# Optimization experiments

Measured on AMD Instinct MI355X. Metric: run time of the kernel, lower is better.

## Reference

```python
import jax, jax.numpy as jnp
import numpy as np

SR = 44100.0
J, Q = 12, 16
W0 = 2.0 * np.pi      # MorletWavelet.freq_to_w_at_s(1.0, s=1.0) -> w = 2*pi*f*s
N_SIG = 3.0           # wavelet support = +/- N_SIG standard deviations


def _make_wavelet_bank():
    """Morlet filter bank: J octaves, Q steps/octave, highest freq = nyquist.
    Returns centered, zero-padded real/imag filter stacks of shape (K, Lmax)."""
    dt = 1.0 / SR
    nyq = SR / 2.0
    wavelets = []
    for j in range(J):
        for q in range(Q):
            f = nyq / (2.0 ** (j + q / Q))
            s = 1.0 / f                      # center freq f = W0/(2*pi*s) = 1/s
            M = int(np.ceil(N_SIG * s * SR))  # half support in samples
            t = np.arange(-M, M + 1) * dt
            psi = (np.pi ** -0.25) / np.sqrt(s) \
                * np.exp(1j * W0 * t / s) * np.exp(-0.5 * (t / s) ** 2)
            psi = psi / np.sum(np.abs(psi))   # L1 normalization
            wavelets.append(psi.astype(np.complex64))
    Lmax = max(len(p) for p in wavelets)       # odd (2*M_max + 1)
    bank = np.zeros((len(wavelets), Lmax), np.complex64)
    for i, p in enumerate(wavelets):
        left = (Lmax - len(p)) // 2            # center-pad each wavelet
        bank[i, left:left + len(p)] = p
    return bank


def setup_inputs() -> dict:
    key = jax.random.key(0)
    x = jax.random.normal(key, (2, 1, 32768), dtype=jnp.float32)
    bank = _make_wavelet_bank()
    return {
        "x": x,
        "filt_real": jnp.asarray(bank.real, dtype=jnp.float32),
        "filt_imag": jnp.asarray(bank.imag, dtype=jnp.float32),
    }


def _scat1d(x, filt_real, filt_imag):
    # x: (B, 1, T); filters: (K, L) with L odd. Equivalent to the torch path:
    # pad input by L//2, cross-correlate (F.conv1d) with each complex wavelet,
    # take the modulus. Done via FFT (same math, efficient for ~47k-tap kernels).
    K, L = filt_real.shape
    B, C, T = x.shape  # C == 1 (squeeze_channels=True)
    P = L // 2
    xp = jnp.pad(x[:, 0, :], ((0, 0), (P, P)))       # (B, T + 2P)
    n_full = xp.shape[-1] + L - 1
    N = 1 << (n_full - 1).bit_length()               # next pow2 FFT size
    X = jnp.fft.rfft(xp, N)                          # (B, N//2+1)
    Gr = jnp.fft.rfft(filt_real[:, ::-1], N)         # flip -> corr via conv
    Gi = jnp.fft.rfft(filt_imag[:, ::-1], N)         # (K, N//2+1)
    lo = L - 1                                       # valid-corr offset
    yr = jnp.fft.irfft(X[:, None, :] * Gr[None], N)[..., lo:lo + T]
    yi = jnp.fft.irfft(X[:, None, :] * Gi[None], N)[..., lo:lo + T]
    return jnp.sqrt(yr * yr + yi * yi)               # (B, K, T) modulus


def reference(x, filt_real, filt_imag):
    return _scat1d(x, filt_real, filt_imag)
```

## Files before the change

### kernel.cpp

```cpp
#include <hip/hip_runtime.h>
#include <math.h>

#define T_LEN   32768
#define NK      192
#define NB      2
#define KDIR    48
#define MAXM    56

struct SParams {
  int m1e[144];
  int voff[144];
  int slot[144];
  int ab[9];
  int jb[10];
};

__device__ __forceinline__ int j2_of_q(int q) {
  return 4 + (q >= 5) + (q >= 10) + (q >= 15);
}

__global__ __launch_bounds__(256) void k_vtab(float* __restrict__ ws, SParams P) {
  int ki = blockIdx.y;
  int slotc = P.slot[ki];
  int M1e = P.m1e[ki];
  float* dst = ws + P.voff[ki];
  int nent = 2 * M1e + 2;
  int k = ki + 48;
  int j = k >> 4, q = k & 15;
  float sig = 2.f * exp2f((float)(16 * j + q) * 0.0625f);
  float s1 = sig * 0.86602540378f;
  float gc = -0.5f / (s1 * s1);
  float om = 6.28318530718f / sig;
  float norm = 1.f / (2.50662827463f * s1 * erff((float)M1e / (1.41421356237f * s1)));
  #pragma unroll
  for (int e0 = 0; e0 < 4; ++e0) {
    int e = blockIdx.x * 1024 + e0 * 256 + threadIdx.x;
    if (e >= slotc) continue;
    if (e >= nent) { dst[2 * e] = 0.f; dst[2 * e + 1] = 0.f; continue; }
    float mm = (float)(e - M1e);
    float g = __expf(gc * mm * mm) * norm;
    float sn, cs; __sincosf(om * mm, &sn, &cs);
    dst[2 * e] = g * cs;
    dst[2 * e + 1] = g * sn;
  }
}

__global__ __launch_bounds__(256) void k_zero(float* __restrict__ ws, int base, int n) {
  int i = blockIdx.x * 256 + threadIdx.x;
  if (i < n) ws[base + i] = 0.f;
}


template<int J, int G, int S, int CH>
__device__ __forceinline__ void deep_path(const float* __restrict__ x,
                                          float* __restrict__ ws, const SParams& P,
                                          int q, int rc, int tid,
                                          float* xs, float* red) {
  constexpr int d = 1 << J;
  constexpr int E = 4096;
  constexpr int W = E + (G - 1) * d + 2;
  const int tile = rc / CH;
  const int chunk = rc % CH;
  const int ki = 16 * (J - 3) + q;
  const int J2 = j2_of_q(q);
  const int M1e = P.m1e[ki];
  const int slot = P.slot[ki];
  const int e_base = chunk * (S * E);
  if (e_base >= slot) return;
  const float* vt = ws + P.voff[ki];
  const int n0 = tile * G;
  const int ubase0 = (n0 - J2) * d - M1e;
  const float* xb0 = x;
  const float* xb1 = x + T_LEN;

  float acc[4 * G];
  #pragma unroll
  for (int i = 0; i < 4 * G; ++i) acc[i] = 0.f;

  #pragma unroll
  for (int s = 0; s < S; ++s) {
    int e0 = e_base + s * E;
    if (e0 >= slot) break;
    int ub = ubase0 + e0;
    if (ub >= T_LEN || ub + W <= 0) continue;
    int Ech = slot - e0; if (Ech > E) Ech = E;
    int Wn = Ech + (G - 1) * d + 2;
    int Wh = (Wn + 1) >> 1;
    for (int i = tid; i < Wh; i += 256) {
      int u0 = ub + 2 * i;
      bool ok = (unsigned)u0 <= (unsigned)(T_LEN - 2);
      int uc = ok ? u0 : 0;
      float2 a = *(const float2*)(xb0 + uc);
      float2 b = *(const float2*)(xb1 + uc);
      float4 w;
      w.x = ok ? a.x : 0.f; w.y = ok ? b.x : 0.f;
      w.z = ok ? a.y : 0.f; w.w = ok ? b.y : 0.f;
      *(float4*)(xs + 4 * i) = w;
    }
    __syncthreads();
    int pend = Ech >> 9;
    const float4* xp0 = (const float4*)xs + tid;
    const float* vte = vt + 2 * e0 + 4 * tid;
    for (int ps = 0; ps < pend; ++ps) {
      float4 v = *(const float4*)(vte + (ps << 10));
      const float4* xp = xp0 + (ps << 8);
      #pragma unroll
      for (int g = 0; g < G; ++g) {
        float4 xv = xp[g * (d >> 1)];
        acc[4 * g + 0] += v.x * xv.x + v.z * xv.z;
        acc[4 * g + 1] += v.y * xv.x + v.w * xv.z;
        acc[4 * g + 2] += v.x * xv.y + v.z * xv.w;
        acc[4 * g + 3] += v.y * xv.y + v.w * xv.w;
      }
    }
    __syncthreads();
  }

  #pragma unroll
  for (int st = 1; st < 64; st <<= 1) {
    #pragma unroll
    for (int i = 0; i < 4 * G; ++i) acc[i] += __shfl_xor(acc[i], st, 64);
  }
  int wv = tid >> 6;
  if ((tid & 63) == 0) {
    #pragma unroll
    for (int gg = 0; gg < G; ++gg)
      *(float4*)(red + wv * 64 + 4 * gg) =
        make_float4(acc[4 * gg], acc[4 * gg + 1], acc[4 * gg + 2], acc[4 * gg + 3]);
  }
  __syncthreads();
  if (tid < 4 * G)
    red[256 + tid] = red[tid] + red[64 + tid] + red[128 + tid] + red[192 + tid];
  __syncthreads();
  if (tid < G) {
    int nidx = n0 + tid;
    int Ncu = (32767 >> J) + 17;
    if (nidx < Ncu) {
      float ar0 = red[256 + 4 * tid], ai0 = red[256 + 4 * tid + 1];
      float ar1 = red[256 + 4 * tid + 2], ai1 = red[256 + 4 * tid + 3];
      float ndf = (float)((nidx - J2) * d);
      float rev = ndf * exp2f(-(float)(16 * (J + 1) + q) * 0.0625f);
      rev -= floorf(rev);
      float sn, cs; __sincosf(rev * 6.28318530718f, &sn, &cs);
      float* ap = ws + P.ab[J - 3] + (q * 2) * Ncu * 2;
      float r0 = ar0 * cs - ai0 * sn, i0 = ar0 * sn + ai0 * cs;
      float r1 = ar1 * cs - ai1 * sn, i1 = ar1 * sn + ai1 * cs;
      if (CH == 1) {
        *(float2*)(ap + 2 * nidx) = make_float2(r0, i0);
        *(float2*)(ap + 2 * (Ncu + nidx)) = make_float2(r1, i1);
      } else {
        atomicAdd(ap + 2 * nidx, r0);
        atomicAdd(ap + 2 * nidx + 1, i0);
        atomicAdd(ap + 2 * (Ncu + nidx), r1);
        atomicAdd(ap + 2 * (Ncu + nidx) + 1, i1);
      }
    }
  }
}

template<int J, int TOUT>
__device__ __forceinline__ void small_path(const float* __restrict__ x,
                                           float* __restrict__ ws, const SParams& P,
                                           int q, int tile, int tid,
                                           float* xs, float* red) {
  constexpr int d = 1 << J;
  const int ki = 16 * (J - 3) + q;
  const int J2 = j2_of_q(q);
  const int M1e = P.m1e[ki];
  const int nent = 2 * M1e + 2;
  const float* vt = ws + P.voff[ki];
  const int Ncu = (32767 >> J) + 17;
  const int o0 = tile * TOUT;
  const int ub = (o0 - J2) * d - M1e;
  const int W = (TOUT - 1) * d + nent;
  const int PS = W + (((W - 1) >> J) << 1) + 4;
  const float* xb0 = x;
  const float* xb1 = x + T_LEN;
  for (int i = tid; i < W; i += 256) {
    int u = ub + i;
    bool ok = (unsigned)u < (unsigned)T_LEN;
    int uc = ok ? u : 0;
    float a = xb0[uc]; a = ok ? a : 0.f;
    float bv = xb1[uc]; bv = ok ? bv : 0.f;
    int ad = i + ((i >> J) << 1);
    xs[ad] = a; xs[PS + ad] = bv;
  }
  __syncthreads();
  int th = (TOUT == 128) ? tid : (tid & 127);
  int o = th & (TOUT - 1);
  int b = th / TOUT;
  int half = (TOUT == 64) ? (tid >> 7) : 0;
  int e_lo = 0, e_hi = nent;
  if (TOUT == 64) {
    int eh = (nent >> 2) << 1;
    if (half) e_lo = eh; else e_hi = eh;
  }
  const float* pl = xs + b * PS;
  int sb = o * d;
  float ar = 0.f, ai = 0.f;
  #pragma unroll 4
  for (int e = e_lo; e < e_hi; e += 2) {
    float4 v = *(const float4*)(vt + 2 * e);
    int s = sb + e;
    float2 xv = *(const float2*)(pl + s + ((s >> J) << 1));
    ar += v.x * xv.x + v.z * xv.y;
    ai += v.y * xv.x + v.w * xv.y;
  }
  if (TOUT == 64) {
    if (tid >= 128) { red[2 * (tid - 128)] = ar; red[2 * (tid - 128) + 1] = ai; }
    __syncthreads();
    if (tid < 128) { ar += red[2 * tid]; ai += red[2 * tid + 1]; }
  }
  if (half == 0 && o0 + o < Ncu && (TOUT == 128 || tid < 128)) {
    int nidx = o0 + o;
    float ndf = (float)((nidx - J2) * d);
    float rev = ndf * exp2f(-(float)(16 * (J + 1) + q) * 0.0625f);
    rev -= floorf(rev);
    float sn, cs; __sincosf(rev * 6.28318530718f, &sn, &cs);
    float* ap = ws + P.ab[J - 3] + (q * 2) * Ncu * 2;
    *(float2*)(ap + 2 * (b * Ncu + nidx)) = make_float2(ar * cs - ai * sn, ar * sn + ai * cs);
  }
}

__global__ __launch_bounds__(256) void k_s1(const float* __restrict__ x,
                                            float* __restrict__ ws, SParams P) {
  __shared__ __align__(16) float xs[12292];
  __shared__ __align__(16) float red[512];
  int bx = blockIdx.x, tid = threadIdx.x;
  int o = 0;
  #pragma unroll
  for (int t = 1; t < 9; ++t) if (bx >= P.jb[t]) o = t;
  int j = 11 - o;
  int rem = bx - P.jb[o];
  int rc = rem >> 4, q = rem & 15;
  switch (j) {
    case 11: deep_path<11, 2, 2, 6>(x, ws, P, q, rc, tid, xs, red); break;
    case 10: deep_path<10, 3, 2, 3>(x, ws, P, q, rc, tid, xs, red); break;
    case 9:  deep_path<9, 4, 1, 3>(x, ws, P, q, rc, tid, xs, red); break;
    case 8:  deep_path<8, 8, 2, 1>(x, ws, P, q, rc, tid, xs, red); break;
    case 7:  deep_path<7, 16, 1, 1>(x, ws, P, q, rc, tid, xs, red); break;
    case 6:  small_path<6, 64>(x, ws, P, q, rc, tid, xs, red); break;
    case 5:  small_path<5, 128>(x, ws, P, q, rc, tid, xs, red); break;
    case 4:  small_path<4, 128>(x, ws, P, q, rc, tid, xs, red); break;
    default: small_path<3, 128>(x, ws, P, q, rc, tid, xs, red); break;
  }
}

__global__ __launch_bounds__(256) void k_stage2(const float* __restrict__ ws,
                                                float* __restrict__ out, SParams P) {
  int k = KDIR + blockIdx.y;
  int j = k >> 4, q = k & 15;
  int d = 1 << j;
  int J2 = j2_of_q(q);
  float sig = 2.f * exp2f((float)(16 * j + q) * 0.0625f);
  float s2 = sig * 0.5f;
  int Ncu = (32767 >> j) + 17;
  const float* A0 = ws + P.ab[j - 3] + (q * 2) * Ncu * 2;
  const float* A1 = A0 + Ncu * 2;
  int t0 = blockIdx.x * 256 + threadIdx.x;
  int phi = t0 & (d - 1);
  int nb0 = t0 >> j;
  int step = 8192 >> j;
  int ntap = 2 * J2 + 1;
  float fd = (float)d;
  float inv2 = 1.f / (s2 * s2);
  float u0 = (float)(phi + J2 * d);
  float eg = __expf(-0.5f * u0 * u0 * inv2);
  float mf = __expf((fd * u0 - 0.5f * fd * fd) * inv2);
  float qf = __expf(-fd * fd * inv2);
  float Z = 0.f;
  float sr0 = 0.f, si0 = 0.f, sr1 = 0.f, si1 = 0.f;
  float sr2 = 0.f, si2 = 0.f, sr3 = 0.f, si3 = 0.f;
  float tr0 = 0.f, ti0 = 0.f, tr1 = 0.f, ti1 = 0.f;
  float tr2 = 0.f, ti2 = 0.f, tr3 = 0.f, ti3 = 0.f;
  const float* Ap0 = A0 + 2 * nb0;
  const float* Ap1 = A1 + 2 * nb0;
  for (int rr = 0; rr < ntap; ++rr) {
    float w = eg; eg *= mf; mf *= qf; Z += w;
    float2 a0 = *(const float2*)(Ap0 + 2 * rr);
    float2 a1 = *(const float2*)(Ap0 + 2 * (rr + step));
    float2 a2 = *(const float2*)(Ap0 + 2 * (rr + 2 * step));
    float2 a3 = *(const float2*)(Ap0 + 2 * (rr + 3 * step));
    float2 b0 = *(const float2*)(Ap1 + 2 * rr);
    float2 b1 = *(const float2*)(Ap1 + 2 * (rr + step));
    float2 b2 = *(const float2*)(Ap1 + 2 * (rr + 2 * step));
    float2 b3 = *(const float2*)(Ap1 + 2 * (rr + 3 * step));
    sr0 += w * a0.x; si0 += w * a0.y; sr1 += w * a1.x; si1 += w * a1.y;
    sr2 += w * a2.x; si2 += w * a2.y; sr3 += w * a3.x; si3 += w * a3.y;
    tr0 += w * b0.x; ti0 += w * b0.y; tr1 += w * b1.x; ti1 += w * b1.y;
    tr2 += w * b2.x; ti2 += w * b2.y; tr3 += w * b3.x; ti3 += w * b3.y;
  }
  float zi = 1.f / Z;
  size_t ob0 = (size_t)k * T_LEN + t0;
  size_t ob1 = (size_t)(NK + k) * T_LEN + t0;
  out[ob0]         = sqrtf(sr0 * sr0 + si0 * si0) * zi;
  out[ob0 + 8192]  = sqrtf(sr1 * sr1 + si1 * si1) * zi;
  out[ob0 + 16384] = sqrtf(sr2 * sr2 + si2 * si2) * zi;
  out[ob0 + 24576] = sqrtf(sr3 * sr3 + si3 * si3) * zi;
  out[ob1]         = sqrtf(tr0 * tr0 + ti0 * ti0) * zi;
  out[ob1 + 8192]  = sqrtf(tr1 * tr1 + ti1 * ti1) * zi;
  out[ob1 + 16384] = sqrtf(tr2 * tr2 + ti2 * ti2) * zi;
  out[ob1 + 24576] = sqrtf(tr3 * tr3 + ti3 * ti3) * zi;
}

__global__ __launch_bounds__(256) void k_direct(const float* __restrict__ x,
                                               const float* __restrict__ fr,
                                               const float* __restrict__ fi,
                                               float* __restrict__ out, int Lmax) {
  int k = blockIdx.y;
  int b = blockIdx.z;
  int t0 = blockIdx.x * 1024;
  int j = k >> 4, q = k & 15;
  int M = (int)ceil(6.0 * exp2((double)j + (double)q * 0.0625)) + 2;
  int P = Lmax >> 1;
  __shared__ __align__(16) float xs[1024 + 2 * MAXM + 4];
  __shared__ __align__(16) float frs[2 * MAXM + 4], fis[2 * MAXM + 4];
  int tid = threadIdx.x;
  int xlen = 1024 + 2 * M;
  const float* xb = x + b * T_LEN;
  for (int i = tid; i < xlen; i += 256) {
    int u = t0 - M + i;
    xs[i] = (u >= 0 && u < T_LEN) ? xb[u] : 0.f;
  }
  if (tid < 4) xs[xlen + tid] = 0.f;
  const float* frk = fr + (size_t)k * Lmax + (P - M);
  const float* fik = fi + (size_t)k * Lmax + (P - M);
  int tl = 2 * M + 1;
  for (int i = tid; i < tl; i += 256) { frs[i] = frk[i]; fis[i] = fik[i]; }
  if (tid < 3) { frs[tl + tid] = 0.f; fis[tl + tid] = 0.f; }
  __syncthreads();
  float ar0 = 0.f, ar1 = 0.f, ar2 = 0.f, ar3 = 0.f;
  float ai0 = 0.f, ai1 = 0.f, ai2 = 0.f, ai3 = 0.f;
  const float4* xsv = (const float4*)(xs + 4 * tid);
  float4 w0 = xsv[0];
  int groups = (tl + 3) >> 2;
  for (int g = 0; g < groups; ++g) {
    float4 w1 = xsv[g + 1];
    float4 f4 = *(const float4*)(frs + 4 * g);
    float4 h4 = *(const float4*)(fis + 4 * g);
    ar0 += f4.x * w0.x + f4.y * w0.y + f4.z * w0.z + f4.w * w0.w;
    ai0 += h4.x * w0.x + h4.y * w0.y + h4.z * w0.z + h4.w * w0.w;
    ar1 += f4.x * w0.y + f4.y * w0.z + f4.z * w0.w + f4.w * w1.x;
    ai1 += h4.x * w0.y + h4.y * w0.z + h4.z * w0.w + h4.w * w1.x;
    ar2 += f4.x * w0.z + f4.y * w0.w + f4.z * w1.x + f4.w * w1.y;
    ai2 += h4.x * w0.z + h4.y * w0.w + h4.z * w1.x + h4.w * w1.y;
    ar3 += f4.x * w0.w + f4.y * w1.x + f4.z * w1.y + f4.w * w1.z;
    ai3 += h4.x * w0.w + h4.y * w1.x + h4.z * w1.y + h4.w * w1.z;
    w0 = w1;
  }
  size_t ob = (size_t)(b * NK + k) * T_LEN + t0 + 4 * tid;
  float4 res;
  res.x = sqrtf(ar0 * ar0 + ai0 * ai0);
  res.y = sqrtf(ar1 * ar1 + ai1 * ai1);
  res.z = sqrtf(ar2 * ar2 + ai2 * ai2);
  res.w = sqrtf(ar3 * ar3 + ai3 * ai3);
  *(float4*)(out + ob) = res;
}

extern "C" void kernel_launch(void* const* d_in, const int* in_sizes, int n_in,
                              void* d_out, int out_size, void* d_ws, size_t ws_size,
                              hipStream_t stream) {
  const float* x  = (const float*)d_in[0];
  const float* fr = (const float*)d_in[1];
  const float* fi = (const float*)d_in[2];
  float* out = (float*)d_out;
  float* ws  = (float*)d_ws;
  int Lmax = in_sizes[1] / NK;

  SParams Pm;
  int cur = 0, maxslot = 0;
  for (int ki = 0; ki < 144; ++ki) {
    int j = (ki + 48) >> 4, q = ki & 15;
    double sig = 2.0 * exp2(((double)(16 * j + q)) / 16.0);
    double s1 = sig * 0.86602540378443864676;
    int M1 = (int)ceil(3.5 * s1);
    int M1e = (M1 + 1) & ~1;
    int slotc = (2 * M1e + 2 + 511) & ~511;
    Pm.m1e[ki] = M1e;
    Pm.voff[ki] = cur;
    Pm.slot[ki] = slotc;
    if (slotc > maxslot) maxslot = slotc;
    cur += 2 * slotc;
  }
  for (int j = 3; j <= 11; ++j) {
    Pm.ab[j - 3] = cur;
    cur += 32 * ((32767 >> j) + 17) * 2;
  }
  const int DG[5]  = {2, 3, 4, 8, 16};
  const int DCH[5] = {6, 3, 3, 1, 1};
  Pm.jb[0] = 0;
  for (int o = 0; o < 9; ++o) {
    int j = 11 - o;
    int Ncu = (32767 >> j) + 17;
    int cnt;
    if (o < 5) {
      int tiles = (Ncu + DG[o] - 1) / DG[o];
      cnt = tiles * DCH[o] * 16;
    } else {
      int TOUT = (j == 6) ? 64 : 128;
      cnt = ((Ncu + TOUT - 1) / TOUT) * 16;
    }
    Pm.jb[o + 1] = Pm.jb[o] + cnt;
  }
  int zbase = Pm.ab[6];
  int zn = (Pm.ab[8] + 32 * ((32767 >> 11) + 17) * 2) - zbase;

  k_vtab<<<dim3((maxslot + 1023) / 1024, 144), dim3(256), 0, stream>>>(ws, Pm);
  k_zero<<<dim3((zn + 255) / 256), dim3(256), 0, stream>>>(ws, zbase, zn);
  k_s1<<<dim3(Pm.jb[9]), dim3(256), 0, stream>>>(x, ws, Pm);
  k_direct<<<dim3(T_LEN / 1024, KDIR, NB), dim3(256), 0, stream>>>(x, fr, fi, out, Lmax);
  k_stage2<<<dim3(T_LEN / (256 * 4), NK - KDIR), dim3(256), 0, stream>>>(ws, out, Pm);
}
```

Before: 251.5 us.

## Fuse direct path into stage-1 kernel and compute deep wavelet taps on the fly

Merges the zeroing and vtab kernels into one prep launch and folds the direct small-filter convolution into the stage-1 kernel as an extra block range, cutting two launches. The deep-octave paths now generate the Gaussian-modulated taps inline with exp and sincos instead of reading a precomputed table, so only the small paths still need one. It also halves the deep chunk size and retunes chunk, split and tile counts, and generalises the small path to split the tap range across several thread segments. This trades table memory traffic for extra transcendental math and rebalances the amount of work per block.

```diff
diff --git a/kernel.cpp b/kernel.cpp
--- a/kernel.cpp
+++ b/kernel.cpp
@@ -9,17 +9,23 @@
 
 struct SParams {
   int m1e[144];
-  int voff[144];
   int slot[144];
+  int voff[64];
   int ab[9];
-  int jb[10];
+  int jb[11];
 };
 
 __device__ __forceinline__ int j2_of_q(int q) {
   return 4 + (q >= 5) + (q >= 10) + (q >= 15);
 }
 
-__global__ __launch_bounds__(256) void k_vtab(float* __restrict__ ws, SParams P) {
+__global__ __launch_bounds__(256) void k_pre(float* __restrict__ ws, SParams P,
+                                             int zbase, int zn) {
+  int tid = threadIdx.x;
+  if (blockIdx.y == 64) {
+    for (int i = blockIdx.x * 256 + tid; i < zn; i += 512) ws[zbase + i] = 0.f;
+    return;
+  }
   int ki = blockIdx.y;
   int slotc = P.slot[ki];
   int M1e = P.m1e[ki];
@@ -34,7 +40,7 @@
   float norm = 1.f / (2.50662827463f * s1 * erff((float)M1e / (1.41421356237f * s1)));
   #pragma unroll
   for (int e0 = 0; e0 < 4; ++e0) {
-    int e = blockIdx.x * 1024 + e0 * 256 + threadIdx.x;
+    int e = blockIdx.x * 1024 + e0 * 256 + tid;
     if (e >= slotc) continue;
     if (e >= nent) { dst[2 * e] = 0.f; dst[2 * e + 1] = 0.f; continue; }
     float mm = (float)(e - M1e);
@@ -45,11 +51,6 @@
   }
 }
 
-__global__ __launch_bounds__(256) void k_zero(float* __restrict__ ws, int base, int n) {
-  int i = blockIdx.x * 256 + threadIdx.x;
-  if (i < n) ws[base + i] = 0.f;
-}
-
 
 template<int J, int G, int S, int CH>
 __device__ __forceinline__ void deep_path(const float* __restrict__ x,
@@ -57,7 +58,7 @@
                                           int q, int rc, int tid,
                                           float* xs, float* red) {
   constexpr int d = 1 << J;
-  constexpr int E = 4096;
+  constexpr int E = 2048;
   constexpr int W = E + (G - 1) * d + 2;
   const int tile = rc / CH;
   const int chunk = rc % CH;
@@ -67,11 +68,16 @@
   const int slot = P.slot[ki];
   const int e_base = chunk * (S * E);
   if (e_base >= slot) return;
-  const float* vt = ws + P.voff[ki];
+  const int nent = 2 * M1e + 2;
   const int n0 = tile * G;
   const int ubase0 = (n0 - J2) * d - M1e;
   const float* xb0 = x;
   const float* xb1 = x + T_LEN;
+  float sig = 2.f * exp2f((float)(16 * J + q) * 0.0625f);
+  float s1 = sig * 0.86602540378f;
+  float gc = -0.5f / (s1 * s1);
+  float om = 6.28318530718f / sig;
+  float norm = 1.f / (2.50662827463f * s1 * erff((float)M1e / (1.41421356237f * s1)));
 
   float acc[4 * G];
   #pragma unroll
@@ -82,9 +88,9 @@
     int e0 = e_base + s * E;
     if (e0 >= slot) break;
     int ub = ubase0 + e0;
-    if (ub >= T_LEN || ub + W <= 0) continue;
     int Ech = slot - e0; if (Ech > E) Ech = E;
     int Wn = Ech + (G - 1) * d + 2;
+    if (ub >= T_LEN || ub + Wn <= 0) continue;
     int Wh = (Wn + 1) >> 1;
     for (int i = tid; i < Wh; i += 256) {
       int u0 = ub + 2 * i;
@@ -100,17 +106,27 @@
     __syncthreads();
     int pend = Ech >> 9;
     const float4* xp0 = (const float4*)xs + tid;
-    const float* vte = vt + 2 * e0 + 4 * tid;
+    int et = e0 + 2 * tid;
     for (int ps = 0; ps < pend; ++ps) {
-      float4 v = *(const float4*)(vte + (ps << 10));
+      int e = et + (ps << 9);
+      float vx, vy, vz, vw;
+      if (e < nent) {
+        float mm0 = (float)(e - M1e), mm1 = mm0 + 1.f;
+        float g0 = __expf(gc * mm0 * mm0) * norm;
+        float g1 = __expf(gc * mm1 * mm1) * norm;
+        float sn0, cs0, sn1, cs1;
+        __sincosf(om * mm0, &sn0, &cs0);
+        __sincosf(om * mm1, &sn1, &cs1);
+        vx = g0 * cs0; vy = g0 * sn0; vz = g1 * cs1; vw = g1 * sn1;
+      } else { vx = 0.f; vy = 0.f; vz = 0.f; vw = 0.f; }
       const float4* xp = xp0 + (ps << 8);
       #pragma unroll
       for (int g = 0; g < G; ++g) {
         float4 xv = xp[g * (d >> 1)];
-        acc[4 * g + 0] += v.x * xv.x + v.z * xv.z;
-        acc[4 * g + 1] += v.y * xv.x + v.w * xv.z;
-        acc[4 * g + 2] += v.x * xv.y + v.z * xv.w;
-        acc[4 * g + 3] += v.y * xv.y + v.w * xv.w;
+        acc[4 * g + 0] += vx * xv.x + vz * xv.z;
+        acc[4 * g + 1] += vy * xv.x + vw * xv.z;
+        acc[4 * g + 2] += vx * xv.y + vz * xv.w;
+        acc[4 * g + 3] += vy * xv.y + vw * xv.w;
       }
     }
     __syncthreads();
@@ -158,12 +174,14 @@
   }
 }
 
-template<int J, int TOUT>
+template<int J, int TOUT, int LT>
 __device__ __forceinline__ void small_path(const float* __restrict__ x,
                                            float* __restrict__ ws, const SParams& P,
                                            int q, int tile, int tid,
                                            float* xs, float* red) {
   constexpr int d = 1 << J;
+  constexpr int TASKS = TOUT * 2;
+  constexpr int SPLIT = 256 / TASKS;
   const int ki = 16 * (J - 3) + q;
   const int J2 = j2_of_q(q);
   const int M1e = P.m1e[ki];
@@ -186,15 +204,12 @@
     xs[ad] = a; xs[PS + ad] = bv;
   }
   __syncthreads();
-  int th = (TOUT == 128) ? tid : (tid & 127);
-  int o = th & (TOUT - 1);
-  int b = th / TOUT;
-  int half = (TOUT == 64) ? (tid >> 7) : 0;
-  int e_lo = 0, e_hi = nent;
-  if (TOUT == 64) {
-    int eh = (nent >> 2) << 1;
-    if (half) e_lo = eh; else e_hi = eh;
-  }
+  int o = tid & (TOUT - 1);
+  int b = (tid >> LT) & 1;
+  int seg = tid >> (LT + 1);
+  int per = ((nent >> 1) + SPLIT - 1) / SPLIT;
+  int e_lo = 2 * per * seg; if (e_lo > nent) e_lo = nent;
+  int e_hi = e_lo + 2 * per; if (e_hi > nent) e_hi = nent;
   const float* pl = xs + b * PS;
   int sb = o * d;
   float ar = 0.f, ai = 0.f;
@@ -206,12 +221,18 @@
     ar += v.x * xv.x + v.z * xv.y;
     ai += v.y * xv.x + v.w * xv.y;
   }
-  if (TOUT == 64) {
-    if (tid >= 128) { red[2 * (tid - 128)] = ar; red[2 * (tid - 128) + 1] = ai; }
+  if (SPLIT > 1) {
+    red[tid] = ar; red[256 + tid] = ai;
     __syncthreads();
-    if (tid < 128) { ar += red[2 * tid]; ai += red[2 * tid + 1]; }
-  }
-  if (half == 0 && o0 + o < Ncu && (TOUT == 128 || tid < 128)) {
+    if (seg == 0) {
+      #pragma unroll
+      for (int ss = 1; ss < SPLIT; ++ss) {
+        ar += red[tid + ss * TASKS];
+        ai += red[256 + tid + ss * TASKS];
+      }
+    }
+  }
+  if (seg == 0 && o0 + o < Ncu) {
     int nidx = o0 + o;
     float ndf = (float)((nidx - J2) * d);
     float rev = ndf * exp2f(-(float)(16 * (J + 1) + q) * 0.0625f);
@@ -222,27 +243,87 @@
   }
 }
 
+__device__ __forceinline__ void direct_path(const float* __restrict__ x,
+                                            const float* __restrict__ fr,
+                                            const float* __restrict__ fi,
+                                            float* __restrict__ out, int Lmax,
+                                            int rem, int tid,
+                                            float* xs, float* red) {
+  int b = rem / 1536;
+  int r2 = rem - b * 1536;
+  int k = r2 >> 5;
+  int t0 = (r2 & 31) << 10;
+  int j = k >> 4, q = k & 15;
+  int M = (int)ceil(6.0 * exp2((double)j + (double)q * 0.0625)) + 2;
+  int P = Lmax >> 1;
+  float* frs = red;
+  float* fis = red + 128;
+  int xlen = 1024 + 2 * M;
+  const float* xb = x + b * T_LEN;
+  for (int i = tid; i < xlen; i += 256) {
+    int u = t0 - M + i;
+    xs[i] = (u >= 0 && u < T_LEN) ? xb[u] : 0.f;
+  }
+  if (tid < 4) xs[xlen + tid] = 0.f;
+  const float* frk = fr + (size_t)k * Lmax + (P - M);
+  const float* fik = fi + (size_t)k * Lmax + (P - M);
+  int tl = 2 * M + 1;
+  for (int i = tid; i < tl; i += 256) { frs[i] = frk[i]; fis[i] = fik[i]; }
+  if (tid < 3) { frs[tl + tid] = 0.f; fis[tl + tid] = 0.f; }
+  __syncthreads();
+  float ar0 = 0.f, ar1 = 0.f, ar2 = 0.f, ar3 = 0.f;
+  float ai0 = 0.f, ai1 = 0.f, ai2 = 0.f, ai3 = 0.f;
+  const float4* xsv = (const float4*)(xs + 4 * tid);
+  float4 w0 = xsv[0];
+  int groups = (tl + 3) >> 2;
+  for (int g = 0; g < groups; ++g) {
+    float4 w1 = xsv[g + 1];
+    float4 f4 = *(const float4*)(frs + 4 * g);
+    float4 h4 = *(const float4*)(fis + 4 * g);
+    ar0 += f4.x * w0.x + f4.y * w0.y + f4.z * w0.z + f4.w * w0.w;
+    ai0 += h4.x * w0.x + h4.y * w0.y + h4.z * w0.z + h4.w * w0.w;
+    ar1 += f4.x * w0.y + f4.y * w0.z + f4.z * w0.w + f4.w * w1.x;
+    ai1 += h4.x * w0.y + h4.y * w0.z + h4.z * w0.w + h4.w * w1.x;
+    ar2 += f4.x * w0.z + f4.y * w0.w + f4.z * w1.x + f4.w * w1.y;
+    ai2 += h4.x * w0.z + h4.y * w0.w + h4.z * w1.x + h4.w * w1.y;
+    ar3 += f4.x * w0.w + f4.y * w1.x + f4.z * w1.y + f4.w * w1.z;
+    ai3 += h4.x * w0.w + h4.y * w1.x + h4.z * w1.y + h4.w * w1.z;
+    w0 = w1;
+  }
+  size_t ob = (size_t)(b * NK + k) * T_LEN + t0 + 4 * tid;
+  float4 res;
+  res.x = sqrtf(ar0 * ar0 + ai0 * ai0);
+  res.y = sqrtf(ar1 * ar1 + ai1 * ai1);
+  res.z = sqrtf(ar2 * ar2 + ai2 * ai2);
+  res.w = sqrtf(ar3 * ar3 + ai3 * ai3);
+  *(float4*)(out + ob) = res;
+}
+
 __global__ __launch_bounds__(256) void k_s1(const float* __restrict__ x,
+                                            const float* __restrict__ fr,
+                                            const float* __restrict__ fi,
+                                            float* __restrict__ out, int Lmax,
                                             float* __restrict__ ws, SParams P) {
-  __shared__ __align__(16) float xs[12292];
+  __shared__ __align__(16) float xs[8196];
   __shared__ __align__(16) float red[512];
   int bx = blockIdx.x, tid = threadIdx.x;
   int o = 0;
   #pragma unroll
-  for (int t = 1; t < 9; ++t) if (bx >= P.jb[t]) o = t;
+  for (int t = 1; t < 10; ++t) if (bx >= P.jb[t]) o = t;
+  int rem = bx - P.jb[o];
+  if (o == 9) { direct_path(x, fr, fi, out, Lmax, rem, tid, xs, red); return; }
   int j = 11 - o;
-  int rem = bx - P.jb[o];
   int rc = rem >> 4, q = rem & 15;
   switch (j) {
-    case 11: deep_path<11, 2, 2, 6>(x, ws, P, q, rc, tid, xs, red); break;
-    case 10: deep_path<10, 3, 2, 3>(x, ws, P, q, rc, tid, xs, red); break;
-    case 9:  deep_path<9, 4, 1, 3>(x, ws, P, q, rc, tid, xs, red); break;
-    case 8:  deep_path<8, 8, 2, 1>(x, ws, P, q, rc, tid, xs, red); break;
-    case 7:  deep_path<7, 16, 1, 1>(x, ws, P, q, rc, tid, xs, red); break;
-    case 6:  small_path<6, 64>(x, ws, P, q, rc, tid, xs, red); break;
-    case 5:  small_path<5, 128>(x, ws, P, q, rc, tid, xs, red); break;
-    case 4:  small_path<4, 128>(x, ws, P, q, rc, tid, xs, red); break;
-    default: small_path<3, 128>(x, ws, P, q, rc, tid, xs, red); break;
+    case 11: deep_path<11, 2, 2, 12>(x, ws, P, q, rc, tid, xs, red); break;
+    case 10: deep_path<10, 3, 2, 6>(x, ws, P, q, rc, tid, xs, red); break;
+    case 9:  deep_path<9, 4, 2, 3>(x, ws, P, q, rc, tid, xs, red); break;
+    case 8:  deep_path<8, 8, 3, 1>(x, ws, P, q, rc, tid, xs, red); break;
+    case 7:  deep_path<7, 16, 2, 1>(x, ws, P, q, rc, tid, xs, red); break;
+    case 6:  small_path<6, 32, 5>(x, ws, P, q, rc, tid, xs, red); break;
+    case 5:  small_path<5, 64, 6>(x, ws, P, q, rc, tid, xs, red); break;
+    case 4:  small_path<4, 128, 7>(x, ws, P, q, rc, tid, xs, red); break;
+    default: small_path<3, 128, 7>(x, ws, P, q, rc, tid, xs, red); break;
   }
 }
 
@@ -303,60 +384,6 @@
   out[ob1 + 24576] = sqrtf(tr3 * tr3 + ti3 * ti3) * zi;
 }
 
-__global__ __launch_bounds__(256) void k_direct(const float* __restrict__ x,
-                                               const float* __restrict__ fr,
-                                               const float* __restrict__ fi,
-                                               float* __restrict__ out, int Lmax) {
-  int k = blockIdx.y;
-  int b = blockIdx.z;
-  int t0 = blockIdx.x * 1024;
-  int j = k >> 4, q = k & 15;
-  int M = (int)ceil(6.0 * exp2((double)j + (double)q * 0.0625)) + 2;
-  int P = Lmax >> 1;
-  __shared__ __align__(16) float xs[1024 + 2 * MAXM + 4];
-  __shared__ __align__(16) float frs[2 * MAXM + 4], fis[2 * MAXM + 4];
-  int tid = threadIdx.x;
-  int xlen = 1024 + 2 * M;
-  const float* xb = x + b * T_LEN;
-  for (int i = tid; i < xlen; i += 256) {
-    int u = t0 - M + i;
-    xs[i] = (u >= 0 && u < T_LEN) ? xb[u] : 0.f;
-  }
-  if (tid < 4) xs[xlen + tid] = 0.f;
-  const float* frk = fr + (size_t)k * Lmax + (P - M);
-  const float* fik = fi + (size_t)k * Lmax + (P - M);
-  int tl = 2 * M + 1;
-  for (int i = tid; i < tl; i += 256) { frs[i] = frk[i]; fis[i] = fik[i]; }
-  if (tid < 3) { frs[tl + tid] = 0.f; fis[tl + tid] = 0.f; }
-  __syncthreads();
-  float ar0 = 0.f, ar1 = 0.f, ar2 = 0.f, ar3 = 0.f;
-  float ai0 = 0.f, ai1 = 0.f, ai2 = 0.f, ai3 = 0.f;
-  const float4* xsv = (const float4*)(xs + 4 * tid);
-  float4 w0 = xsv[0];
-  int groups = (tl + 3) >> 2;
-  for (int g = 0; g < groups; ++g) {
-    float4 w1 = xsv[g + 1];
-    float4 f4 = *(const float4*)(frs + 4 * g);
-    float4 h4 = *(const float4*)(fis + 4 * g);
-    ar0 += f4.x * w0.x + f4.y * w0.y + f4.z * w0.z + f4.w * w0.w;
-    ai0 += h4.x * w0.x + h4.y * w0.y + h4.z * w0.z + h4.w * w0.w;
-    ar1 += f4.x * w0.y + f4.y * w0.z + f4.z * w0.w + f4.w * w1.x;
-    ai1 += h4.x * w0.y + h4.y * w0.z + h4.z * w0.w + h4.w * w1.x;
-    ar2 += f4.x * w0.z + f4.y * w0.w + f4.z * w1.x + f4.w * w1.y;
-    ai2 += h4.x * w0.z + h4.y * w0.w + h4.z * w1.x + h4.w * w1.y;
-    ar3 += f4.x * w0.w + f4.y * w1.x + f4.z * w1.y + f4.w * w1.z;
-    ai3 += h4.x * w0.w + h4.y * w1.x + h4.z * w1.y + h4.w * w1.z;
-    w0 = w1;
-  }
-  size_t ob = (size_t)(b * NK + k) * T_LEN + t0 + 4 * tid;
-  float4 res;
-  res.x = sqrtf(ar0 * ar0 + ai0 * ai0);
-  res.y = sqrtf(ar1 * ar1 + ai1 * ai1);
-  res.z = sqrtf(ar2 * ar2 + ai2 * ai2);
-  res.w = sqrtf(ar3 * ar3 + ai3 * ai3);
-  *(float4*)(out + ob) = res;
-}
-
 extern "C" void kernel_launch(void* const* d_in, const int* in_sizes, int n_in,
                               void* d_out, int out_size, void* d_ws, size_t ws_size,
                               hipStream_t stream) {
@@ -368,7 +395,7 @@
   int Lmax = in_sizes[1] / NK;
 
   SParams Pm;
-  int cur = 0, maxslot = 0;
+  int cur = 0;
   for (int ki = 0; ki < 144; ++ki) {
     int j = (ki + 48) >> 4, q = ki & 15;
     double sig = 2.0 * exp2(((double)(16 * j + q)) / 16.0);
@@ -377,17 +404,19 @@
     int M1e = (M1 + 1) & ~1;
     int slotc = (2 * M1e + 2 + 511) & ~511;
     Pm.m1e[ki] = M1e;
-    Pm.voff[ki] = cur;
     Pm.slot[ki] = slotc;
-    if (slotc > maxslot) maxslot = slotc;
-    cur += 2 * slotc;
+    if (ki < 64) {
+      Pm.voff[ki] = cur;
+      cur += 2 * slotc;
+    }
   }
   for (int j = 3; j <= 11; ++j) {
     Pm.ab[j - 3] = cur;
     cur += 32 * ((32767 >> j) + 17) * 2;
   }
   const int DG[5]  = {2, 3, 4, 8, 16};
-  const int DCH[5] = {6, 3, 3, 1, 1};
+  const int DCH[5] = {12, 6, 3, 1, 1};
+  const int STO[4] = {32, 64, 128, 128};
   Pm.jb[0] = 0;
   for (int o = 0; o < 9; ++o) {
     int j = 11 - o;
@@ -397,17 +426,17 @@
       int tiles = (Ncu + DG[o] - 1) / DG[o];
       cnt = tiles * DCH[o] * 16;
     } else {
-      int TOUT = (j == 6) ? 64 : 128;
+      int TOUT = STO[o - 5];
       cnt = ((Ncu + TOUT - 1) / TOUT) * 16;
     }
     Pm.jb[o + 1] = Pm.jb[o] + cnt;
   }
+  Pm.jb[10] = Pm.jb[9] + (T_LEN / 1024) * KDIR * NB;
+
   int zbase = Pm.ab[6];
   int zn = (Pm.ab[8] + 32 * ((32767 >> 11) + 17) * 2) - zbase;
 
-  k_vtab<<<dim3((maxslot + 1023) / 1024, 144), dim3(256), 0, stream>>>(ws, Pm);
-  k_zero<<<dim3((zn + 255) / 256), dim3(256), 0, stream>>>(ws, zbase, zn);
-  k_s1<<<dim3(Pm.jb[9]), dim3(256), 0, stream>>>(x, ws, Pm);
-  k_direct<<<dim3(T_LEN / 1024, KDIR, NB), dim3(256), 0, stream>>>(x, fr, fi, out, Lmax);
+  k_pre<<<dim3(2, 65), dim3(256), 0, stream>>>(ws, Pm, zbase, zn);
+  k_s1<<<dim3(Pm.jb[10]), dim3(256), 0, stream>>>(x, fr, fi, out, Lmax, ws, Pm);
   k_stage2<<<dim3(T_LEN / (256 * 4), NK - KDIR), dim3(256), 0, stream>>>(ws, out, Pm);
 }
```

Result: slower. 257.5 us (+2.4%).
